# Kernel optimization log

Hardware: AMD Instinct MI355X
Metric: run time of the kernel (lower is better)

The kernel has to match this reference:

```python
import jax, jax.numpy as jnp
import numpy as np
from jax import lax


def setup_inputs() -> dict:
    key = jax.random.key(0)
    k1, k2, k3, k4 = jax.random.split(key, 4)
    B, K, Hp, Wp = 512, 64, 5, 5
    num_classes = 10
    x = jax.random.uniform(k1, (B, 1, 20, 20), dtype=jnp.float32)
    patterns = jax.random.uniform(k2, (K, 1, Hp, Wp), dtype=jnp.float32)
    w2 = jax.random.normal(k3, (1, K), dtype=jnp.float32) * 0.1
    b2 = jnp.zeros((1,), dtype=jnp.float32)
    wf = jax.random.normal(k4, (num_classes, 400), dtype=jnp.float32) * 0.05
    bf = jnp.zeros((num_classes,), dtype=jnp.float32)
    return {"x": x, "patterns": patterns, "w2": w2, "b2": b2, "wf": wf, "bf": bf}


def _geneo1(patterns, x):
    # patterns: (K,1,Hp,Wp), x: (B,1,H,W). Same-padded sliding L1 similarity.
    K, _, Hp, Wp = patterns.shape
    P = Hp * Wp
    xp = jnp.pad(x, ((0, 0), (0, 0), (Hp // 2, Hp // 2), (Wp // 2, Wp // 2)))
    # (B, P, H_out, W_out); C=1 so feature order is row-major over (Hp,Wp),
    # matching torch's unfold(2,Hp,1).unfold(3,Wp,1).reshape(-1).
    patches = lax.conv_general_dilated_patches(xp, (Hp, Wp), (1, 1), "VALID")
    pat = patterns.reshape(K, P)
    # (B,K,H_out,W_out): mean_|p| |pattern - patch|
    diff = jnp.abs(pat[None, :, :, None, None] - patches[:, None, :, :, :]).mean(axis=2)
    return 1.0 - diff


def _channel_wise_max(t):
    B, K, H, W = t.shape
    flat = t.reshape(B, K, H * W)
    idx = jnp.argmax(flat, axis=2)                      # (B,K)
    mask = jax.nn.one_hot(idx, H * W, dtype=flat.dtype) # (B,K,HW)
    return (flat * mask).reshape(B, K, H, W)


def reference(x, patterns, w2, b2, wf, bf):
    Fk = _geneo1(patterns, x)            # (B,K,20,20)
    cwm = _channel_wise_max(Fk)          # (B,K,20,20)
    # GENEO2: Linear(K,1) over channel dim (applied on (B,H,W,K))
    t = jnp.einsum("bkhw,ok->bhwo", cwm, w2) + b2   # (B,20,20,1)
    t = jax.nn.sigmoid(t)
    out = t.reshape(t.shape[0], -1) @ wf.T + bf      # (B,num_classes)
    return jax.nn.sigmoid(out)
```

## Files before the change

### kernel.cpp

```cpp
#include <hip/hip_runtime.h>
#include <math.h>

#define NB 512
#define NK 64
#define NP 25
#define HW 400
#define NC 10

__device__ __forceinline__ unsigned sad16(unsigned a, unsigned b, unsigned c) {
#if __has_builtin(__builtin_amdgcn_sad_u16)
    return __builtin_amdgcn_sad_u16(a, b, c);
#else
    unsigned d;
    asm("v_sad_u16 %0, %1, %2, %3" : "=v"(d) : "v"(a), "v"(b), "v"(c));
    return d;
#endif
}

__global__ void geneo_mlp_kernel(
    const float* __restrict__ x,
    const float* __restrict__ patterns,
    const float* __restrict__ w2,
    const float* __restrict__ b2,
    const float* __restrict__ wf,
    const float* __restrict__ bf,
    float* __restrict__ out)
{
    __shared__ unsigned xq[24 * 24];
    __shared__ unsigned pqd[23 * 24];
    __shared__ __align__(16) float pat_lds[NK * NP];
    __shared__ unsigned redbest[4][NK];
    __shared__ float2 contrib[NK];
    __shared__ float  wsum[4][NC];

    const int tid  = threadIdx.x;
    const int b    = blockIdx.x;
    const int lane = tid & 63;
    const int wave = tid >> 6;

    for (int i = tid; i < 576; i += 256) {
        const int h = i / 24, w = i - h * 24;
        float v = 0.f;
        if (h >= 2 && h < 22 && w >= 2 && w < 22)
            v = x[b * HW + (h - 2) * 20 + (w - 2)];
        xq[i] = (unsigned)(v * 65535.f + 0.5f);
    }
    {
        const float4* p4 = reinterpret_cast<const float4*>(patterns);
        float4*       l4 = reinterpret_cast<float4*>(pat_lds);
        l4[tid] = p4[tid];
        if (tid + 256 < 400) l4[tid + 256] = p4[tid + 256];
    }
    __syncthreads();

    for (int i = tid; i < 552; i += 256)
        pqd[i] = xq[i] | (xq[i + 24] << 16);

    unsigned vp01[5], vp23[5], p4v[5];
    #pragma unroll
    for (int c = 0; c < 5; ++c) {
        const unsigned q0 = (unsigned)(pat_lds[lane * NP +  0 + c] * 65535.f + 0.5f);
        const unsigned q1 = (unsigned)(pat_lds[lane * NP +  5 + c] * 65535.f + 0.5f);
        const unsigned q2 = (unsigned)(pat_lds[lane * NP + 10 + c] * 65535.f + 0.5f);
        const unsigned q3 = (unsigned)(pat_lds[lane * NP + 15 + c] * 65535.f + 0.5f);
        const unsigned q4 = (unsigned)(pat_lds[lane * NP + 20 + c] * 65535.f + 0.5f);
        vp01[c] = q0 | (q1 << 16);
        vp23[c] = q2 | (q3 << 16);
        p4v[c]  = q4;
    }
    __syncthreads();

    unsigned best = 0xFFFFFFFFu;
    const int h0 = wave * 5;

    #pragma unroll 1
    for (int r = 0; r < 5; ++r) {
        const int h = h0 + r;
        #pragma unroll 1
        for (int cb = 0; cb < 4; ++cb) {
            const int c0 = cb * 5;
            const unsigned* r01 = &pqd[h * 24 + c0];
            const unsigned* r23 = &pqd[(h + 2) * 24 + c0];
            const unsigned* r4  = &xq[(h + 4) * 24 + c0];
            unsigned W01[9], W23[9], W4[9];
            #pragma unroll
            for (int d = 0; d < 9; ++d) {
                W01[d] = r01[d]; W23[d] = r23[d]; W4[d] = r4[d];
            }
            #pragma unroll
            for (int px = 0; px < 5; ++px) {
                unsigned s = 0;
                #pragma unroll
                for (int dx = 0; dx < 5; ++dx) {
                    s = sad16(W01[px + dx], vp01[dx], s);
                    s = sad16(W23[px + dx], vp23[dx], s);
                    s = sad16(W4 [px + dx], p4v [dx], s);
                }
                const unsigned pk = (s << 9) | (unsigned)(h * 20 + c0 + px);
                best = min(best, pk);
            }
        }
    }
    redbest[wave][lane] = best;
    __syncthreads();

    if (tid < NK) {
        const unsigned b0 = min(min(redbest[0][tid], redbest[1][tid]),
                                min(redbest[2][tid], redbest[3][tid]));
        const unsigned s  = b0 >> 9;
        const int    pix  = (int)(b0 & 511u);
        const float  F    = 1.f - (float)s * (1.f / (25.f * 65535.f));
        contrib[tid] = make_float2(F * w2[tid], __int_as_float(pix));
    }
    __syncthreads();

    float acc[NC];
    #pragma unroll
    for (int c = 0; c < NC; ++c) acc[c] = 0.f;
    const float b2v = b2[0];

    {
        const int p0 = tid;
        float s = b2v;
        for (int k = 0; k < NK; ++k) {
            const float2 cv = contrib[k];
            if (__float_as_int(cv.y) == p0) s += cv.x;
        }
        const float t = 1.f / (1.f + expf(-s));
        #pragma unroll
        for (int c = 0; c < NC; ++c) acc[c] += t * wf[c * HW + p0];
    }
    if (tid + 256 < HW) {
        const int p1 = tid + 256;
        float s = b2v;
        for (int k = 0; k < NK; ++k) {
            const float2 cv = contrib[k];
            if (__float_as_int(cv.y) == p1) s += cv.x;
        }
        const float t = 1.f / (1.f + expf(-s));
        #pragma unroll
        for (int c = 0; c < NC; ++c) acc[c] += t * wf[c * HW + p1];
    }

    #pragma unroll
    for (int c = 0; c < NC; ++c) {
        #pragma unroll
        for (int off = 32; off >= 1; off >>= 1)
            acc[c] += __shfl_down(acc[c], off);
    }
    if (lane == 0) {
        #pragma unroll
        for (int c = 0; c < NC; ++c) wsum[wave][c] = acc[c];
    }
    __syncthreads();
    if (tid < NC) {
        const float s = wsum[0][tid] + wsum[1][tid] + wsum[2][tid] + wsum[3][tid] + bf[tid];
        out[b * NC + tid] = 1.f / (1.f + expf(-s));
    }
}

extern "C" void kernel_launch(void* const* d_in, const int* in_sizes, int n_in,
                              void* d_out, int out_size, void* d_ws, size_t ws_size,
                              hipStream_t stream) {
    const float* x        = (const float*)d_in[0];
    const float* patterns = (const float*)d_in[1];
    const float* w2       = (const float*)d_in[2];
    const float* b2       = (const float*)d_in[3];
    const float* wf       = (const float*)d_in[4];
    const float* bf       = (const float*)d_in[5];
    float* out = (float*)d_out;

    geneo_mlp_kernel<<<NB, 256, 0, stream>>>(x, patterns, w2, b2, wf, bf, out);
}
```

Measured before the change: 23.09 us.

## Split SAD scan across 16 waves per block with 1024-thread blocks

Raises the block size from 256 to 1024 threads so each of 16 waves scans a 5x5 tile of output positions instead of 5 rows by 20 columns. Each wave does a quarter of the previous SAD work, shortening the per-block critical path, since 512 blocks of 4 waves left the GPU lightly occupied. In exchange, the cross-wave min reduction and the final class sum now combine 16 partials instead of 4. The setup and MLP phases now use one thread per element, and a large block adds barrier cost.

```diff
diff --git a/kernel.cpp b/kernel.cpp
--- a/kernel.cpp
+++ b/kernel.cpp
@@ -6,6 +6,7 @@
 #define NP 25
 #define HW 400
 #define NC 10
+#define NWAVE 16
 
 __device__ __forceinline__ unsigned sad16(unsigned a, unsigned b, unsigned c) {
 #if __has_builtin(__builtin_amdgcn_sad_u16)
@@ -17,7 +18,7 @@
 #endif
 }
 
-__global__ void geneo_mlp_kernel(
+__global__ __launch_bounds__(1024, 4) void geneo_mlp_kernel(
     const float* __restrict__ x,
     const float* __restrict__ patterns,
     const float* __restrict__ w2,
@@ -29,32 +30,29 @@
     __shared__ unsigned xq[24 * 24];
     __shared__ unsigned pqd[23 * 24];
     __shared__ __align__(16) float pat_lds[NK * NP];
-    __shared__ unsigned redbest[4][NK];
+    __shared__ unsigned redbest[NWAVE][NK];
     __shared__ float2 contrib[NK];
-    __shared__ float  wsum[4][NC];
+    __shared__ float  wsum[NWAVE][NC];
 
     const int tid  = threadIdx.x;
     const int b    = blockIdx.x;
     const int lane = tid & 63;
     const int wave = tid >> 6;
 
-    for (int i = tid; i < 576; i += 256) {
-        const int h = i / 24, w = i - h * 24;
+    if (tid < 576) {
+        const int h = tid / 24, w = tid - h * 24;
         float v = 0.f;
         if (h >= 2 && h < 22 && w >= 2 && w < 22)
             v = x[b * HW + (h - 2) * 20 + (w - 2)];
-        xq[i] = (unsigned)(v * 65535.f + 0.5f);
+        xq[tid] = (unsigned)(v * 65535.f + 0.5f);
     }
-    {
-        const float4* p4 = reinterpret_cast<const float4*>(patterns);
-        float4*       l4 = reinterpret_cast<float4*>(pat_lds);
-        l4[tid] = p4[tid];
-        if (tid + 256 < 400) l4[tid + 256] = p4[tid + 256];
-    }
+    if (tid < 400)
+        reinterpret_cast<float4*>(pat_lds)[tid] =
+            reinterpret_cast<const float4*>(patterns)[tid];
     __syncthreads();
 
-    for (int i = tid; i < 552; i += 256)
-        pqd[i] = xq[i] | (xq[i + 24] << 16);
+    if (tid < 552)
+        pqd[tid] = xq[tid] | (xq[tid + 24] << 16);
 
     unsigned vp01[5], vp23[5], p4v[5];
     #pragma unroll
@@ -70,43 +68,42 @@
     }
     __syncthreads();
 
+    const int tr = wave >> 2;
+    const int tc = wave & 3;
+    const int c0 = tc * 5;
     unsigned best = 0xFFFFFFFFu;
-    const int h0 = wave * 5;
 
     #pragma unroll 1
     for (int r = 0; r < 5; ++r) {
-        const int h = h0 + r;
-        #pragma unroll 1
-        for (int cb = 0; cb < 4; ++cb) {
-            const int c0 = cb * 5;
-            const unsigned* r01 = &pqd[h * 24 + c0];
-            const unsigned* r23 = &pqd[(h + 2) * 24 + c0];
-            const unsigned* r4  = &xq[(h + 4) * 24 + c0];
-            unsigned W01[9], W23[9], W4[9];
+        const int h = tr * 5 + r;
+        const unsigned* r01 = &pqd[h * 24 + c0];
+        const unsigned* r23 = &pqd[(h + 2) * 24 + c0];
+        const unsigned* r4  = &xq[(h + 4) * 24 + c0];
+        unsigned W01[9], W23[9], W4[9];
+        #pragma unroll
+        for (int d = 0; d < 9; ++d) {
+            W01[d] = r01[d]; W23[d] = r23[d]; W4[d] = r4[d];
+        }
+        #pragma unroll
+        for (int px = 0; px < 5; ++px) {
+            unsigned s = 0;
             #pragma unroll
-            for (int d = 0; d < 9; ++d) {
-                W01[d] = r01[d]; W23[d] = r23[d]; W4[d] = r4[d];
+            for (int dx = 0; dx < 5; ++dx) {
+                s = sad16(W01[px + dx], vp01[dx], s);
+                s = sad16(W23[px + dx], vp23[dx], s);
+                s = sad16(W4 [px + dx], p4v [dx], s);
             }
-            #pragma unroll
-            for (int px = 0; px < 5; ++px) {
-                unsigned s = 0;
-                #pragma unroll
-                for (int dx = 0; dx < 5; ++dx) {
-                    s = sad16(W01[px + dx], vp01[dx], s);
-                    s = sad16(W23[px + dx], vp23[dx], s);
-                    s = sad16(W4 [px + dx], p4v [dx], s);
-                }
-                const unsigned pk = (s << 9) | (unsigned)(h * 20 + c0 + px);
-                best = min(best, pk);
-            }
+            const unsigned pk = (s << 9) | (unsigned)(h * 20 + c0 + px);
+            best = min(best, pk);
         }
     }
     redbest[wave][lane] = best;
     __syncthreads();
 
     if (tid < NK) {
-        const unsigned b0 = min(min(redbest[0][tid], redbest[1][tid]),
-                                min(redbest[2][tid], redbest[3][tid]));
+        unsigned b0 = redbest[0][tid];
+        #pragma unroll
+        for (int w = 1; w < NWAVE; ++w) b0 = min(b0, redbest[w][tid]);
         const unsigned s  = b0 >> 9;
         const int    pix  = (int)(b0 & 511u);
         const float  F    = 1.f - (float)s * (1.f / (25.f * 65535.f));
@@ -117,29 +114,17 @@
     float acc[NC];
     #pragma unroll
     for (int c = 0; c < NC; ++c) acc[c] = 0.f;
-    const float b2v = b2[0];
 
-    {
-        const int p0 = tid;
-        float s = b2v;
+    if (tid < HW) {
+        float s = b2[0];
+        #pragma unroll 8
         for (int k = 0; k < NK; ++k) {
             const float2 cv = contrib[k];
-            if (__float_as_int(cv.y) == p0) s += cv.x;
+            if (__float_as_int(cv.y) == tid) s += cv.x;
         }
         const float t = 1.f / (1.f + expf(-s));
         #pragma unroll
-        for (int c = 0; c < NC; ++c) acc[c] += t * wf[c * HW + p0];
-    }
-    if (tid + 256 < HW) {
-        const int p1 = tid + 256;
-        float s = b2v;
-        for (int k = 0; k < NK; ++k) {
-            const float2 cv = contrib[k];
-            if (__float_as_int(cv.y) == p1) s += cv.x;
-        }
-        const float t = 1.f / (1.f + expf(-s));
-        #pragma unroll
-        for (int c = 0; c < NC; ++c) acc[c] += t * wf[c * HW + p1];
+        for (int c = 0; c < NC; ++c) acc[c] += t * wf[c * HW + tid];
     }
 
     #pragma unroll
@@ -154,7 +139,9 @@
     }
     __syncthreads();
     if (tid < NC) {
-        const float s = wsum[0][tid] + wsum[1][tid] + wsum[2][tid] + wsum[3][tid] + bf[tid];
+        float s = bf[tid];
+        #pragma unroll
+        for (int w = 0; w < NWAVE; ++w) s += wsum[w][tid];
         out[b * NC + tid] = 1.f / (1.f + expf(-s));
     }
 }
@@ -170,5 +157,5 @@
     const float* bf       = (const float*)d_in[5];
     float* out = (float*)d_out;
 
-    geneo_mlp_kernel<<<NB, 256, 0, stream>>>(x, patterns, w2, b2, wf, bf, out);
+    geneo_mlp_kernel<<<NB, 1024, 0, stream>>>(x, patterns, w2, b2, wf, bf, out);
 }
```

Measured after the change: 21.51 us. 1.07x faster.
